# Kernel optimization log

Hardware: AMD Instinct MI355X
Metric: run time of the kernel (lower is better)

## Reference

```python
import jax, jax.numpy as jnp
import numpy as np
from numpy.polynomial import Polynomial

B, C = 2000000, 10
EXP = dict(start=0.0, stop=1.0, n=1000, deg=8)
INV = dict(start=10.0, stop=30.0, n=1000, deg=4)
LOG = dict(start=0.01, stop=0.5, n=1000, deg=8)
ITERATIONS = 3


def _fit(fn, start, stop, n, deg):
    x = np.linspace(start, stop, n)
    return Polynomial.fit(x, fn(x), deg).convert(kind=Polynomial).coef.astype(np.float32)


def _polyval(coeffs, x):
    # Horner; coeffs ascending order (numpy Polynomial convention)
    res = jnp.full_like(x, coeffs[-1])
    for i in range(coeffs.shape[0] - 2, -1, -1):
        res = res * x + coeffs[i]
    return res


def setup_inputs() -> dict:
    key = jax.random.key(0)
    k1, k2 = jax.random.split(key)
    enc_input = jax.random.uniform(k1, (B, C), dtype=jnp.float32)  # logits in [0,1)
    labels = jax.random.randint(k2, (B,), 0, C)
    enc_target = jax.nn.one_hot(labels, C, dtype=jnp.float32)
    exp_coeffs = jnp.asarray(_fit(np.exp, **{'start': EXP['start'], 'stop': EXP['stop'], 'n': EXP['n'], 'deg': EXP['deg']}))
    inverse_coeffs = jnp.asarray(_fit(lambda x: 1.0 / x, INV['start'], INV['stop'], INV['n'], INV['deg']))
    log_coeffs = jnp.asarray(_fit(np.log, LOG['start'], LOG['stop'], LOG['n'], LOG['deg']))
    return {
        'enc_input': enc_input,
        'enc_target': enc_target,
        'exp_coeffs': exp_coeffs,
        'inverse_coeffs': inverse_coeffs,
        'log_coeffs': log_coeffs,
        'iterations': ITERATIONS,
    }


def reference(enc_input, enc_target, exp_coeffs, inverse_coeffs, log_coeffs, iterations):
    # exp via polynomial approximation (Horner / ciphertext poly eval)
    e = _polyval(exp_coeffs, enc_input)                      # [B, C]
    s = jnp.sum(e, axis=1, keepdims=True)                    # [B, 1]
    # inverse via polynomial initial guess + Newton-Raphson refinement
    inv = _polyval(inverse_coeffs, s)
    for _ in range(iterations):
        inv = inv * (2.0 - s * inv)
    softmax = e * inv                                        # [B, C]
    log_softmax = _polyval(log_coeffs, softmax)              # [B, C]
    # mean cross-entropy over the batch
    loss = -jnp.sum(enc_target * log_softmax) / enc_input.shape[0]
    return loss


if __name__ == '__main__':
    out = reference(**setup_inputs())
    print(out)
```

## Files before the change

### kernel.cpp

```cpp
#include <hip/hip_runtime.h>

#define CCOL 10
#define TPB 256
#define PAIR_BYTES 80
#define WAVE_BYTES (64 * PAIR_BYTES)
#define CHUNK_LD 1024
#define NBLOCKS 768

typedef const __attribute__((address_space(1))) void* gptr_t;
typedef __attribute__((address_space(3))) void* lptr_t;

__global__ __launch_bounds__(TPB) void ce_kernel(
    const float* __restrict__ x, const float* __restrict__ tgt,
    const float* __restrict__ exp_c, const float* __restrict__ inv_c,
    const float* __restrict__ log_c, const int* __restrict__ iters_p,
    float* __restrict__ partials, int npairs, int full_chunks, int total_chunks)
{
    __shared__ float sx[TPB * 2 * CCOL];
    __shared__ float st[TPB * 2 * CCOL];

    float ec[9], ic[5], lc[9];
#pragma unroll
    for (int i = 0; i < 9; i++) ec[i] = exp_c[i];
#pragma unroll
    for (int i = 0; i < 5; i++) ic[i] = inv_c[i];
#pragma unroll
    for (int i = 0; i < 9; i++) lc[i] = log_c[i];
    const int niter = iters_p[0];

    const int tid  = threadIdx.x;
    const int lane = tid & 63;
    const int w    = tid >> 6;

    float local = 0.0f;

    for (int c = blockIdx.x; c < total_chunks; c += gridDim.x) {
        const int pair0 = c * TPB;
        float xr[2 * CCOL], tr[2 * CCOL];
        bool have = false;

        if (c < full_chunks) {
            const char* gx = (const char*)x   + (size_t)pair0 * PAIR_BYTES + w * WAVE_BYTES + lane * 16;
            const char* gt = (const char*)tgt + (size_t)pair0 * PAIR_BYTES + w * WAVE_BYTES + lane * 16;
            char* lx = (char*)sx + w * WAVE_BYTES + lane * 16;
            char* lt = (char*)st + w * WAVE_BYTES + lane * 16;
#pragma unroll
            for (int i = 0; i < 5; i++)
                __builtin_amdgcn_global_load_lds((gptr_t)(gx + i * CHUNK_LD), (lptr_t)(lx + i * CHUNK_LD), 16, 0, 0);
#pragma unroll
            for (int i = 0; i < 5; i++)
                __builtin_amdgcn_global_load_lds((gptr_t)(gt + i * CHUNK_LD), (lptr_t)(lt + i * CHUNK_LD), 16, 0, 0);
            __syncthreads();

            const float4* xv = (const float4*)(sx + tid * 2 * CCOL);
            const float4* tv = (const float4*)(st + tid * 2 * CCOL);
#pragma unroll
            for (int i = 0; i < 5; i++) {
                float4 v = xv[i];
                xr[4 * i + 0] = v.x; xr[4 * i + 1] = v.y;
                xr[4 * i + 2] = v.z; xr[4 * i + 3] = v.w;
            }
#pragma unroll
            for (int i = 0; i < 5; i++) {
                float4 v = tv[i];
                tr[4 * i + 0] = v.x; tr[4 * i + 1] = v.y;
                tr[4 * i + 2] = v.z; tr[4 * i + 3] = v.w;
            }
            __syncthreads();
            have = true;
        } else {
            int p = pair0 + tid;
            if (p < npairs) {
                const float4* xv = (const float4*)(x   + (size_t)p * 2 * CCOL);
                const float4* tv = (const float4*)(tgt + (size_t)p * 2 * CCOL);
#pragma unroll
                for (int i = 0; i < 5; i++) {
                    float4 v = xv[i];
                    xr[4 * i + 0] = v.x; xr[4 * i + 1] = v.y;
                    xr[4 * i + 2] = v.z; xr[4 * i + 3] = v.w;
                }
#pragma unroll
                for (int i = 0; i < 5; i++) {
                    float4 v = tv[i];
                    tr[4 * i + 0] = v.x; tr[4 * i + 1] = v.y;
                    tr[4 * i + 2] = v.z; tr[4 * i + 3] = v.w;
                }
                have = true;
            }
        }

        if (have) {
#pragma unroll
            for (int r = 0; r < 2; r++) {
                float e[CCOL];
                float s = 0.0f;
#pragma unroll
                for (int cc = 0; cc < CCOL; cc++) {
                    float xx = xr[r * CCOL + cc];
                    float v = ec[8];
#pragma unroll
                    for (int i = 7; i >= 0; i--) v = fmaf(v, xx, ec[i]);
                    e[cc] = v;
                    s += v;
                }
                float inv = ic[4];
#pragma unroll
                for (int i = 3; i >= 0; i--) inv = fmaf(inv, s, ic[i]);
                for (int k = 0; k < niter; k++) inv = inv * (2.0f - s * inv);

#pragma unroll
                for (int cc = 0; cc < CCOL; cc++) {
                    float sm = e[cc] * inv;
                    float v = lc[8];
#pragma unroll
                    for (int i = 7; i >= 0; i--) v = fmaf(v, sm, lc[i]);
                    local = fmaf(tr[r * CCOL + cc], v, local);
                }
            }
        }
    }

#pragma unroll
    for (int off = 32; off > 0; off >>= 1)
        local += __shfl_down(local, off, 64);

    __shared__ float wsum[4];
    if (lane == 0) wsum[w] = local;
    __syncthreads();
    if (tid == 0)
        partials[blockIdx.x] = wsum[0] + wsum[1] + wsum[2] + wsum[3];
}

__global__ __launch_bounds__(TPB) void reduce_kernel(
    const float* __restrict__ partials, float* __restrict__ out, float neg_inv_b)
{
    int tid = threadIdx.x;
    float local = partials[tid] + partials[tid + 256] + partials[tid + 512];
#pragma unroll
    for (int off = 32; off > 0; off >>= 1)
        local += __shfl_down(local, off, 64);
    __shared__ float wsum[4];
    if ((tid & 63) == 0) wsum[tid >> 6] = local;
    __syncthreads();
    if (tid == 0)
        out[0] = (wsum[0] + wsum[1] + wsum[2] + wsum[3]) * neg_inv_b;
}

extern "C" void kernel_launch(void* const* d_in, const int* in_sizes, int n_in,
                              void* d_out, int out_size, void* d_ws, size_t ws_size,
                              hipStream_t stream) {
    const float* x  = (const float*)d_in[0];
    const float* t  = (const float*)d_in[1];
    const float* ec = (const float*)d_in[2];
    const float* ic = (const float*)d_in[3];
    const float* lc = (const float*)d_in[4];
    const int*   it = (const int*)d_in[5];
    float* out = (float*)d_out;
    float* partials = (float*)d_ws;

    int b_rows = in_sizes[0] / CCOL;
    int npairs = b_rows / 2;
    float neg_inv_b = -1.0f / (float)b_rows;

    int full_chunks  = npairs / TPB;
    int total_chunks = full_chunks + (npairs % TPB ? 1 : 0);

    ce_kernel<<<NBLOCKS, TPB, 0, stream>>>(x, t, ec, ic, lc, it, partials,
                                           npairs, full_chunks, total_chunks);
    reduce_kernel<<<1, TPB, 0, stream>>>(partials, out, neg_inv_b);
}
```

Measured before the change: 185.2 us.

## Per-wave register prefetch pipeline replacing block-synced LDS async loads

Each wave now owns a 64-pair chunk and stages it through its own LDS region. The next chunk is prefetched into registers while the current one is transposed through LDS and computed, which removes the block-wide __syncthreads and the global_load_lds path. The grid grows to 1024 blocks with a launch-bounds occupancy hint, the leftover pairs go through a grid-stride tail loop, and the reduce kernel is generalised to NBLOCKS partials. The trade-off is higher register pressure from the prefetch buffers.

```diff
diff --git a/kernel.cpp b/kernel.cpp
--- a/kernel.cpp
+++ b/kernel.cpp
@@ -2,22 +2,49 @@
 
 #define CCOL 10
 #define TPB 256
-#define PAIR_BYTES 80
-#define WAVE_BYTES (64 * PAIR_BYTES)
-#define CHUNK_LD 1024
-#define NBLOCKS 768
+#define NBLOCKS 1024
 
-typedef const __attribute__((address_space(1))) void* gptr_t;
-typedef __attribute__((address_space(3))) void* lptr_t;
+__device__ __forceinline__ float pair_loss(const float* xr, const float* tr,
+                                           const float* ec, const float* ic,
+                                           const float* lc, int niter)
+{
+    float local = 0.0f;
+#pragma unroll
+    for (int r = 0; r < 2; r++) {
+        float e[CCOL];
+        float s = 0.0f;
+#pragma unroll
+        for (int c = 0; c < CCOL; c++) {
+            float xx = xr[r * CCOL + c];
+            float v = ec[8];
+#pragma unroll
+            for (int i = 7; i >= 0; i--) v = fmaf(v, xx, ec[i]);
+            e[c] = v;
+            s += v;
+        }
+        float inv = ic[4];
+#pragma unroll
+        for (int i = 3; i >= 0; i--) inv = fmaf(inv, s, ic[i]);
+        for (int k = 0; k < niter; k++) inv = inv * (2.0f - s * inv);
+#pragma unroll
+        for (int c = 0; c < CCOL; c++) {
+            float sm = e[c] * inv;
+            float v = lc[8];
+#pragma unroll
+            for (int i = 7; i >= 0; i--) v = fmaf(v, sm, lc[i]);
+            local = fmaf(tr[r * CCOL + c], v, local);
+        }
+    }
+    return local;
+}
 
-__global__ __launch_bounds__(TPB) void ce_kernel(
+__global__ __launch_bounds__(TPB, 4) void ce_kernel(
     const float* __restrict__ x, const float* __restrict__ tgt,
     const float* __restrict__ exp_c, const float* __restrict__ inv_c,
     const float* __restrict__ log_c, const int* __restrict__ iters_p,
-    float* __restrict__ partials, int npairs, int full_chunks, int total_chunks)
+    float* __restrict__ partials, int npairs, int nchunks)
 {
-    __shared__ float sx[TPB * 2 * CCOL];
-    __shared__ float st[TPB * 2 * CCOL];
+    __shared__ float4 lds4[2560];
 
     float ec[9], ic[5], lc[9];
 #pragma unroll
@@ -31,100 +58,84 @@
     const int tid  = threadIdx.x;
     const int lane = tid & 63;
     const int w    = tid >> 6;
+    const int wg   = blockIdx.x * 4 + w;
+    const int W    = gridDim.x * 4;
+
+    float4* lx = lds4 + w * 640;
+    float4* lt = lx + 320;
 
     float local = 0.0f;
 
-    for (int c = blockIdx.x; c < total_chunks; c += gridDim.x) {
-        const int pair0 = c * TPB;
-        float xr[2 * CCOL], tr[2 * CCOL];
-        bool have = false;
+    int q = wg;
+    float4 rx[5], rt[5];
+    if (q < nchunks) {
+        const float4* gx = (const float4*)x   + (size_t)q * 320;
+        const float4* gt = (const float4*)tgt + (size_t)q * 320;
+#pragma unroll
+        for (int i = 0; i < 5; i++) rx[i] = gx[i * 64 + lane];
+#pragma unroll
+        for (int i = 0; i < 5; i++) rt[i] = gt[i * 64 + lane];
+    }
 
-        if (c < full_chunks) {
-            const char* gx = (const char*)x   + (size_t)pair0 * PAIR_BYTES + w * WAVE_BYTES + lane * 16;
-            const char* gt = (const char*)tgt + (size_t)pair0 * PAIR_BYTES + w * WAVE_BYTES + lane * 16;
-            char* lx = (char*)sx + w * WAVE_BYTES + lane * 16;
-            char* lt = (char*)st + w * WAVE_BYTES + lane * 16;
+    while (q < nchunks) {
 #pragma unroll
-            for (int i = 0; i < 5; i++)
-                __builtin_amdgcn_global_load_lds((gptr_t)(gx + i * CHUNK_LD), (lptr_t)(lx + i * CHUNK_LD), 16, 0, 0);
+        for (int i = 0; i < 5; i++) lx[i * 64 + lane] = rx[i];
 #pragma unroll
-            for (int i = 0; i < 5; i++)
-                __builtin_amdgcn_global_load_lds((gptr_t)(gt + i * CHUNK_LD), (lptr_t)(lt + i * CHUNK_LD), 16, 0, 0);
-            __syncthreads();
+        for (int i = 0; i < 5; i++) lt[i * 64 + lane] = rt[i];
 
-            const float4* xv = (const float4*)(sx + tid * 2 * CCOL);
-            const float4* tv = (const float4*)(st + tid * 2 * CCOL);
+        int qn = q + W;
+        if (qn < nchunks) {
+            const float4* gx = (const float4*)x   + (size_t)qn * 320;
+            const float4* gt = (const float4*)tgt + (size_t)qn * 320;
 #pragma unroll
-            for (int i = 0; i < 5; i++) {
-                float4 v = xv[i];
-                xr[4 * i + 0] = v.x; xr[4 * i + 1] = v.y;
-                xr[4 * i + 2] = v.z; xr[4 * i + 3] = v.w;
-            }
+            for (int i = 0; i < 5; i++) rx[i] = gx[i * 64 + lane];
 #pragma unroll
-            for (int i = 0; i < 5; i++) {
-                float4 v = tv[i];
-                tr[4 * i + 0] = v.x; tr[4 * i + 1] = v.y;
-                tr[4 * i + 2] = v.z; tr[4 * i + 3] = v.w;
-            }
-            __syncthreads();
-            have = true;
-        } else {
-            int p = pair0 + tid;
-            if (p < npairs) {
-                const float4* xv = (const float4*)(x   + (size_t)p * 2 * CCOL);
-                const float4* tv = (const float4*)(tgt + (size_t)p * 2 * CCOL);
+            for (int i = 0; i < 5; i++) rt[i] = gt[i * 64 + lane];
+        }
+        __builtin_amdgcn_sched_barrier(0);
+
+        float xr[20], tr[20];
+        const float4* px = (const float4*)((const float*)lx + lane * 20);
+        const float4* pt = (const float4*)((const float*)lt + lane * 20);
 #pragma unroll
-                for (int i = 0; i < 5; i++) {
-                    float4 v = xv[i];
-                    xr[4 * i + 0] = v.x; xr[4 * i + 1] = v.y;
-                    xr[4 * i + 2] = v.z; xr[4 * i + 3] = v.w;
-                }
+        for (int i = 0; i < 5; i++) {
+            float4 v = px[i];
+            xr[4 * i] = v.x; xr[4 * i + 1] = v.y; xr[4 * i + 2] = v.z; xr[4 * i + 3] = v.w;
+        }
 #pragma unroll
-                for (int i = 0; i < 5; i++) {
-                    float4 v = tv[i];
-                    tr[4 * i + 0] = v.x; tr[4 * i + 1] = v.y;
-                    tr[4 * i + 2] = v.z; tr[4 * i + 3] = v.w;
-                }
-                have = true;
-            }
+        for (int i = 0; i < 5; i++) {
+            float4 v = pt[i];
+            tr[4 * i] = v.x; tr[4 * i + 1] = v.y; tr[4 * i + 2] = v.z; tr[4 * i + 3] = v.w;
         }
 
-        if (have) {
+        local += pair_loss(xr, tr, ec, ic, lc, niter);
+        q = qn;
+    }
+
+    int tail0 = nchunks * 64;
+    for (int p = tail0 + blockIdx.x * TPB + tid; p < npairs; p += gridDim.x * TPB) {
+        float xr[20], tr[20];
+        const float4* xv = (const float4*)(x   + (size_t)p * 2 * CCOL);
+        const float4* tv = (const float4*)(tgt + (size_t)p * 2 * CCOL);
 #pragma unroll
-            for (int r = 0; r < 2; r++) {
-                float e[CCOL];
-                float s = 0.0f;
+        for (int i = 0; i < 5; i++) {
+            float4 v = xv[i];
+            xr[4 * i] = v.x; xr[4 * i + 1] = v.y; xr[4 * i + 2] = v.z; xr[4 * i + 3] = v.w;
+        }
 #pragma unroll
-                for (int cc = 0; cc < CCOL; cc++) {
-                    float xx = xr[r * CCOL + cc];
-                    float v = ec[8];
-#pragma unroll
-                    for (int i = 7; i >= 0; i--) v = fmaf(v, xx, ec[i]);
-                    e[cc] = v;
-                    s += v;
-                }
-                float inv = ic[4];
-#pragma unroll
-                for (int i = 3; i >= 0; i--) inv = fmaf(inv, s, ic[i]);
-                for (int k = 0; k < niter; k++) inv = inv * (2.0f - s * inv);
-
-#pragma unroll
-                for (int cc = 0; cc < CCOL; cc++) {
-                    float sm = e[cc] * inv;
-                    float v = lc[8];
-#pragma unroll
-                    for (int i = 7; i >= 0; i--) v = fmaf(v, sm, lc[i]);
-                    local = fmaf(tr[r * CCOL + cc], v, local);
-                }
-            }
+        for (int i = 0; i < 5; i++) {
+            float4 v = tv[i];
+            tr[4 * i] = v.x; tr[4 * i + 1] = v.y; tr[4 * i + 2] = v.z; tr[4 * i + 3] = v.w;
         }
+        local += pair_loss(xr, tr, ec, ic, lc, niter);
     }
 
 #pragma unroll
     for (int off = 32; off > 0; off >>= 1)
         local += __shfl_down(local, off, 64);
 
-    __shared__ float wsum[4];
+    __syncthreads();
+    float* wsum = (float*)lds4;
     if (lane == 0) wsum[w] = local;
     __syncthreads();
     if (tid == 0)
@@ -135,7 +146,10 @@
     const float* __restrict__ partials, float* __restrict__ out, float neg_inv_b)
 {
     int tid = threadIdx.x;
-    float local = partials[tid] + partials[tid + 256] + partials[tid + 512];
+    float local = 0.0f;
+#pragma unroll
+    for (int k = 0; k < NBLOCKS / TPB; k++)
+        local += partials[tid + k * TPB];
 #pragma unroll
     for (int off = 32; off > 0; off >>= 1)
         local += __shfl_down(local, off, 64);
@@ -160,12 +174,10 @@
 
     int b_rows = in_sizes[0] / CCOL;
     int npairs = b_rows / 2;
+    int nchunks = npairs / 64;
     float neg_inv_b = -1.0f / (float)b_rows;
 
-    int full_chunks  = npairs / TPB;
-    int total_chunks = full_chunks + (npairs % TPB ? 1 : 0);
-
     ce_kernel<<<NBLOCKS, TPB, 0, stream>>>(x, t, ec, ic, lc, it, partials,
-                                           npairs, full_chunks, total_chunks);
+                                           npairs, nchunks);
     reduce_kernel<<<1, TPB, 0, stream>>>(partials, out, neg_inv_b);
 }
```

New measurement: 210.9 us. +13.9%, slower.
